# Kernel optimization log

Hardware: AMD Instinct MI355X
Metric: run time of the kernel (lower is better)

## Reference

```python
import jax, jax.numpy as jnp
import numpy as np

B, S, D, H = 2, 2048, 1024, 16
DK = D // H


def setup_inputs() -> dict:
    key = jax.random.key(0)
    ks = jax.random.split(key, 12)
    scale = 0.02
    inp = {
        "query": jax.random.normal(ks[0], (B, S, D), jnp.float32),
        "key_": jax.random.normal(ks[1], (B, S, D), jnp.float32),
        "value": jax.random.normal(ks[2], (B, S, D), jnp.float32),
        # causal mask; masked_fill where mask == 0
        "mask": jnp.tril(jnp.ones((S, S), jnp.int32))[None, None, :, :],
        # torch Linear weights are [out, in]; y = x @ W.T + b
        "Wq": jax.random.normal(ks[3], (D, D), jnp.float32) * scale,
        "bq": jax.random.normal(ks[4], (D,), jnp.float32) * scale,
        "Wk": jax.random.normal(ks[5], (D, D), jnp.float32) * scale,
        "bk": jax.random.normal(ks[6], (D,), jnp.float32) * scale,
        "Wv": jax.random.normal(ks[7], (D, D), jnp.float32) * scale,
        "bv": jax.random.normal(ks[8], (D,), jnp.float32) * scale,
        "Wo": jax.random.normal(ks[9], (D, D), jnp.float32) * scale,
        "bo": jax.random.normal(ks[10], (D,), jnp.float32) * scale,
    }
    return inp


def reference(query, key_, value, mask, Wq, bq, Wk, bk, Wv, bv, Wo, bo):
    # projections (torch Linear: x @ W.T + b)
    Q = query @ Wq.T + bq
    K = key_ @ Wk.T + bk
    V = value @ Wv.T + bv
    # [B, S, D] -> [B, H, S, DK]
    Q = Q.reshape(B, S, H, DK).transpose(0, 2, 1, 3)
    K = K.reshape(B, S, H, DK).transpose(0, 2, 1, 3)
    V = V.reshape(B, S, H, DK).transpose(0, 2, 1, 3)
    scores = jnp.einsum("bhqd,bhkd->bhqk", Q, K) / jnp.sqrt(jnp.float32(DK))
    scores = jnp.where(mask == 0, jnp.float32(-1e9), scores)
    attn = jax.nn.softmax(scores, axis=-1)
    # dropout is identity in eval mode
    context = jnp.einsum("bhqk,bhkd->bhqd", attn, V)
    context = context.transpose(0, 2, 1, 3).reshape(B, S, D)
    output = context @ Wo.T + bo
    return (output, attn)
```

## Files before the change

### kernel.cpp

```cpp
#include <hip/hip_runtime.h>
#include <hip/hip_bf16.h>

#define BB 2
#define SS 2048
#define DD 1024
#define HH 16

typedef __attribute__((ext_vector_type(8))) short bf16x8;
typedef __attribute__((ext_vector_type(4))) float f32x4;
typedef __attribute__((ext_vector_type(4))) unsigned int u32x4;

__device__ inline unsigned short f2bf(float f) {
  unsigned int u = __float_as_uint(f);
  u += 0x7fff + ((u >> 16) & 1);
  return (unsigned short)(u >> 16);
}

__device__ inline void gll16(const void* g, void* l) {
  __builtin_amdgcn_global_load_lds(
      (const __attribute__((address_space(1))) unsigned int*)g,
      (__attribute__((address_space(3))) unsigned int*)l, 16, 0, 0);
}

__device__ inline int swz(int row, int col) {
  return row * 64 + ((((col >> 3) + row + (row >> 3)) & 7) << 3) + (col & 7);
}

__global__ void convert_all(const float* __restrict__ q, const float* __restrict__ k,
                            const float* __restrict__ v, const float* __restrict__ wq,
                            const float* __restrict__ wk, const float* __restrict__ wv,
                            const float* __restrict__ wo, unsigned short* __restrict__ dst) {
  int gi = blockIdx.x * 256 + threadIdx.x;
  long base = (long)gi * 4;
  if (base >= 16777216L) return;
  const float* src;
  long off;
  if (base < 12582912L) {
    int a = (int)(base >> 22);
    off = base & 4194303L;
    src = (a == 0) ? q : (a == 1 ? k : v);
  } else {
    long wb = base - 12582912L;
    int a = (int)(wb >> 20);
    off = wb & 1048575L;
    src = (a == 0) ? wq : (a == 1 ? wk : (a == 2 ? wv : wo));
  }
  const float4 f = *(const float4*)(src + off);
  ushort4 o;
  o.x = f2bf(f.x); o.y = f2bf(f.y); o.z = f2bf(f.z); o.w = f2bf(f.w);
  *(ushort4*)(dst + base) = o;
}

template <int OUT_F32>
__global__ __launch_bounds__(256, 3) void gemm_bt(const unsigned short* __restrict__ Aall,
                                                  const unsigned short* __restrict__ Wall,
                                                  const float* __restrict__ b0,
                                                  const float* __restrict__ b1,
                                                  const float* __restrict__ b2,
                                                  void* __restrict__ Call) {
  __shared__ unsigned short As[128 * 64];
  __shared__ unsigned short Bs[128 * 64];
  const int tid = threadIdx.x;
  const int lane = tid & 63;
  const int w = tid >> 6;
  const int wm = w >> 1, wn = w & 1;
  const int z = blockIdx.z;
  const int m0 = blockIdx.y * 128;
  const int n0 = blockIdx.x * 128;
  const unsigned short* A = Aall + (long)z * 4194304;
  const unsigned short* W = Wall + (long)z * 1048576;
  const float* bias = (z == 0) ? b0 : (z == 1 ? b1 : b2);
  const int r = lane & 15, g = lane >> 4;
  const int lrow = lane >> 3;
  const int lcol = (lane & 7) * 8;

  f32x4 acc[4][4];
#pragma unroll
  for (int i = 0; i < 4; i++)
#pragma unroll
    for (int j = 0; j < 4; j++) acc[i][j] = (f32x4){0.f, 0.f, 0.f, 0.f};

  for (int kt = 0; kt < 16; kt++) {
    const int k0 = kt * 64;
#pragma unroll
    for (int t = 0; t < 4; t++) {
      int row = w * 32 + t * 8 + lrow;
      gll16(A + (long)(m0 + row) * 1024 + k0 + lcol, &As[(w * 32 + t * 8) * 64]);
      gll16(W + (long)(n0 + row) * 1024 + k0 + lcol, &Bs[(w * 32 + t * 8) * 64]);
    }
    __syncthreads();
#pragma unroll
    for (int kk = 0; kk < 2; kk++) {
      bf16x8 af[4], bfr[4];
#pragma unroll
      for (int mi = 0; mi < 4; mi++)
        af[mi] = *(const bf16x8*)&As[(wm * 64 + mi * 16 + r) * 64 + kk * 32 + g * 8];
#pragma unroll
      for (int ni = 0; ni < 4; ni++)
        bfr[ni] = *(const bf16x8*)&Bs[(wn * 64 + ni * 16 + r) * 64 + kk * 32 + g * 8];
#pragma unroll
      for (int mi = 0; mi < 4; mi++)
#pragma unroll
        for (int ni = 0; ni < 4; ni++)
          acc[mi][ni] = __builtin_amdgcn_mfma_f32_16x16x32_bf16(af[mi], bfr[ni], acc[mi][ni], 0, 0, 0);
    }
    __syncthreads();
  }
#pragma unroll
  for (int ni = 0; ni < 4; ni++) {
    int n = n0 + wn * 64 + ni * 16 + r;
    float bv = bias[n];
#pragma unroll
    for (int mi = 0; mi < 4; mi++) {
#pragma unroll
      for (int reg = 0; reg < 4; reg++) {
        int m = m0 + wm * 64 + mi * 16 + g * 4 + reg;
        float val = acc[mi][ni][reg] + bv;
        if (OUT_F32)
          ((float*)Call)[(long)m * 1024 + n] = val;
        else
          ((unsigned short*)Call)[(long)z * 4194304 + (long)m * 1024 + n] = f2bf(val);
      }
    }
  }
}

__global__ __launch_bounds__(256, 3) void attn_kernel(const unsigned short* __restrict__ Qb,
                                                      const unsigned short* __restrict__ Kb,
                                                      const unsigned short* __restrict__ Vb,
                                                      unsigned short* __restrict__ Ctx,
                                                      float* __restrict__ attn) {
  __shared__ unsigned short Qs[64 * 64];
  __shared__ unsigned short Ks[2][64 * 64];
  __shared__ unsigned short Vt[2][64 * 64];
  __shared__ unsigned short Ps[64 * 64];
  const int tid = threadIdx.x;
  const int lane = tid & 63;
  const int w = tid >> 6;
  const int r = lane & 15, g = lane >> 4;
  const int h = blockIdx.y, b = blockIdx.z;
  const int bh = b * HH + h;
  const unsigned short* Kg = Kb + (long)b * SS * DD + h * 64;
  const unsigned short* Vg = Vb + (long)b * SS * DD + h * 64;
  float* attn_bh = attn + (long)bh * SS * SS;
  const int srow = tid >> 3;
  const int scg = tid & 7;

  for (int half = 0; half < 2; half++) {
    const int qt = half ? (31 - (int)blockIdx.x) : (int)blockIdx.x;
    const int q0 = qt * 64;
    const unsigned short* Qg = Qb + (long)(b * SS + q0) * DD + h * 64;

    __syncthreads();
    u32x4 kpre[2];
#pragma unroll
    for (int it = 0; it < 2; it++) {
      int row = it * 32 + srow;
      *(u32x4*)&Qs[swz(row, scg * 8)] = *(const u32x4*)(Qg + (long)row * DD + scg * 8);
      kpre[it] = *(const u32x4*)(Kg + (long)row * DD + scg * 8);
    }
    __syncthreads();
    bf16x8 aq0 = *(const bf16x8*)&Qs[swz(16 * w + r, g * 8)];
    bf16x8 aq1 = *(const bf16x8*)&Qs[swz(16 * w + r, 32 + g * 8)];

    float rs[4] = {0.f, 0.f, 0.f, 0.f};
    for (int kt = 0; kt <= qt; kt++) {
      unsigned short* kbuf = Ks[kt & 1];
#pragma unroll
      for (int it = 0; it < 2; it++)
        *(u32x4*)&kbuf[swz(it * 32 + srow, scg * 8)] = kpre[it];
      const int ktn = (kt < qt) ? kt + 1 : kt;
#pragma unroll
      for (int it = 0; it < 2; it++)
        kpre[it] = *(const u32x4*)(Kg + (long)(ktn * 64 + it * 32 + srow) * DD + scg * 8);
      __syncthreads();
#pragma unroll
      for (int tj = 0; tj < 4; tj++) {
        bf16x8 bk0 = *(const bf16x8*)&kbuf[swz(tj * 16 + r, g * 8)];
        bf16x8 bk1 = *(const bf16x8*)&kbuf[swz(tj * 16 + r, 32 + g * 8)];
        f32x4 sa = (f32x4){0.f, 0.f, 0.f, 0.f};
        sa = __builtin_amdgcn_mfma_f32_16x16x32_bf16(aq0, bk0, sa, 0, 0, 0);
        sa = __builtin_amdgcn_mfma_f32_16x16x32_bf16(aq1, bk1, sa, 0, 0, 0);
        int colb = kt * 64 + tj * 16 + r;
        int rowb = q0 + 16 * w + g * 4;
#pragma unroll
        for (int reg = 0; reg < 4; reg++) {
          float p = (colb <= rowb + reg) ? __expf(sa[reg] * 0.125f) : 0.f;
          rs[reg] += p;
        }
      }
    }
#pragma unroll
    for (int reg = 0; reg < 4; reg++) {
#pragma unroll
      for (int m = 1; m <= 8; m <<= 1) rs[reg] += __shfl_xor(rs[reg], m);
    }
    float inv[4];
#pragma unroll
    for (int reg = 0; reg < 4; reg++) inv[reg] = 1.f / rs[reg];

    f32x4 oacc[4];
#pragma unroll
    for (int dj = 0; dj < 4; dj++) oacc[dj] = (f32x4){0.f, 0.f, 0.f, 0.f};
    u32x4 vpre[2];
#pragma unroll
    for (int it = 0; it < 2; it++) {
      int row = it * 32 + srow;
      kpre[it] = *(const u32x4*)(Kg + (long)row * DD + scg * 8);
      vpre[it] = *(const u32x4*)(Vg + (long)row * DD + scg * 8);
    }
    __syncthreads();
    for (int kt = 0; kt <= qt; kt++) {
      unsigned short* kbuf = Ks[kt & 1];
      unsigned short* vbuf = Vt[kt & 1];
#pragma unroll
      for (int it = 0; it < 2; it++) {
        *(u32x4*)&kbuf[swz(it * 32 + srow, scg * 8)] = kpre[it];
        union { u32x4 v4; unsigned short s[8]; } uv;
        uv.v4 = vpre[it];
#pragma unroll
        for (int i = 0; i < 8; i++) vbuf[swz(scg * 8 + i, it * 32 + srow)] = uv.s[i];
      }
      const int ktn = (kt < qt) ? kt + 1 : kt;
#pragma unroll
      for (int it = 0; it < 2; it++) {
        kpre[it] = *(const u32x4*)(Kg + (long)(ktn * 64 + it * 32 + srow) * DD + scg * 8);
        vpre[it] = *(const u32x4*)(Vg + (long)(ktn * 64 + it * 32 + srow) * DD + scg * 8);
      }
      __syncthreads();
#pragma unroll
      for (int tj = 0; tj < 4; tj++) {
        bf16x8 bk0 = *(const bf16x8*)&kbuf[swz(tj * 16 + r, g * 8)];
        bf16x8 bk1 = *(const bf16x8*)&kbuf[swz(tj * 16 + r, 32 + g * 8)];
        f32x4 sa = (f32x4){0.f, 0.f, 0.f, 0.f};
        sa = __builtin_amdgcn_mfma_f32_16x16x32_bf16(aq0, bk0, sa, 0, 0, 0);
        sa = __builtin_amdgcn_mfma_f32_16x16x32_bf16(aq1, bk1, sa, 0, 0, 0);
        int colb = kt * 64 + tj * 16 + r;
        int rowl = 16 * w + g * 4;
#pragma unroll
        for (int reg = 0; reg < 4; reg++) {
          int rowg = q0 + rowl + reg;
          float p = (colb <= rowg) ? __expf(sa[reg] * 0.125f) * inv[reg] : 0.f;
          attn_bh[(long)rowg * SS + colb] = p;
          Ps[swz(rowl + reg, tj * 16 + r)] = f2bf(p);
        }
      }
#pragma unroll
      for (int kk = 0; kk < 2; kk++) {
        bf16x8 ap = *(const bf16x8*)&Ps[swz(16 * w + r, kk * 32 + g * 8)];
#pragma unroll
        for (int dj = 0; dj < 4; dj++) {
          bf16x8 bv = *(const bf16x8*)&vbuf[swz(dj * 16 + r, kk * 32 + g * 8)];
          oacc[dj] = __builtin_amdgcn_mfma_f32_16x16x32_bf16(ap, bv, oacc[dj], 0, 0, 0);
        }
      }
    }
#pragma unroll
    for (int dj = 0; dj < 4; dj++) {
#pragma unroll
      for (int reg = 0; reg < 4; reg++) {
        int rowg = q0 + 16 * w + g * 4 + reg;
        Ctx[(long)(b * SS + rowg) * DD + h * 64 + dj * 16 + r] = f2bf(oacc[dj][reg]);
      }
    }
    int zs = (qt + 1) * 64;
    if (zs < SS) {
      int zc = SS - zs;
      f32x4 zero = (f32x4){0.f, 0.f, 0.f, 0.f};
      for (int rr = 0; rr < 64; rr++) {
        float* rp = attn_bh + (long)(q0 + rr) * SS + zs;
        for (int cc = tid * 4; cc < zc; cc += 1024) *(f32x4*)(rp + cc) = zero;
      }
    }
  }
}

extern "C" void kernel_launch(void* const* d_in, const int* in_sizes, int n_in,
                              void* d_out, int out_size, void* d_ws, size_t ws_size,
                              hipStream_t stream) {
  const float* q  = (const float*)d_in[0];
  const float* k  = (const float*)d_in[1];
  const float* v  = (const float*)d_in[2];
  const float* wq = (const float*)d_in[4];
  const float* bq = (const float*)d_in[5];
  const float* wk = (const float*)d_in[6];
  const float* bk = (const float*)d_in[7];
  const float* wv = (const float*)d_in[8];
  const float* bv = (const float*)d_in[9];
  const float* wo = (const float*)d_in[10];
  const float* bo = (const float*)d_in[11];

  unsigned short* ws = (unsigned short*)d_ws;
  unsigned short* Xq  = ws;
  unsigned short* Wqb = ws + 12582912;
  unsigned short* Qb  = ws + 16777216;
  unsigned short* Ctx = ws + 29360128;
  float* outp = (float*)d_out;
  float* attn = outp + 4194304;

  convert_all<<<dim3(16384), dim3(256), 0, stream>>>(q, k, v, wq, wk, wv, wo, ws);
  gemm_bt<0><<<dim3(8, 32, 3), dim3(256), 0, stream>>>(Xq, Wqb, bq, bk, bv, (void*)Qb);
  attn_kernel<<<dim3(16, 16, 2), dim3(256), 0, stream>>>(Qb, Qb + 4194304, Qb + 8388608, Ctx, attn);
  gemm_bt<1><<<dim3(8, 32, 1), dim3(256), 0, stream>>>(Ctx, Wqb + 3145728, bo, bo, bo, (void*)outp);
}
```

Baseline: 778.6 us.

## Compute transposed scores, load K/V straight from global, pre-transpose V in projection

The V projection epilogue now writes V transposed per batch-head, so the attention kernel can read V^T fragments directly from global memory. K and Q tiles are also read directly from global into MFMA operands, removing the LDS staging, double buffering and most barriers. Scores are computed as K·Q^T so each lane owns one query row; this makes the attention-probability stores contiguous float4 writes and turns the row-sum reduction into two shuffles. The costs are more uncached global traffic for repeated K/V reads, a lower occupancy hint in launch bounds, and no apparent barrier around the Ps reuse across iterations.

Result: slower. 858.6 us (+10.3%).

```diff
diff --git a/kernel.cpp b/kernel.cpp
--- a/kernel.cpp
+++ b/kernel.cpp
@@ -9,6 +9,7 @@
 typedef __attribute__((ext_vector_type(8))) short bf16x8;
 typedef __attribute__((ext_vector_type(4))) float f32x4;
 typedef __attribute__((ext_vector_type(4))) unsigned int u32x4;
+typedef __attribute__((ext_vector_type(2))) unsigned int u32x2;
 
 __device__ inline unsigned short f2bf(float f) {
   unsigned int u = __float_as_uint(f);
@@ -112,27 +113,38 @@
     float bv = bias[n];
 #pragma unroll
     for (int mi = 0; mi < 4; mi++) {
-#pragma unroll
-      for (int reg = 0; reg < 4; reg++) {
-        int m = m0 + wm * 64 + mi * 16 + g * 4 + reg;
-        float val = acc[mi][ni][reg] + bv;
-        if (OUT_F32)
-          ((float*)Call)[(long)m * 1024 + n] = val;
-        else
-          ((unsigned short*)Call)[(long)z * 4194304 + (long)m * 1024 + n] = f2bf(val);
-      }
-    }
-  }
-}
-
-__global__ __launch_bounds__(256, 3) void attn_kernel(const unsigned short* __restrict__ Qb,
+      if (OUT_F32) {
+#pragma unroll
+        for (int reg = 0; reg < 4; reg++) {
+          int m = m0 + wm * 64 + mi * 16 + g * 4 + reg;
+          ((float*)Call)[(long)m * 1024 + n] = acc[mi][ni][reg] + bv;
+        }
+      } else if (z == 2) {
+        int m = m0 + wm * 64 + mi * 16 + g * 4;
+        ushort4 o;
+        o.x = f2bf(acc[mi][ni][0] + bv);
+        o.y = f2bf(acc[mi][ni][1] + bv);
+        o.z = f2bf(acc[mi][ni][2] + bv);
+        o.w = f2bf(acc[mi][ni][3] + bv);
+        long idx = 2L * 4194304 + ((long)((m >> 11) * 1024 + n)) * 2048 + (m & 2047);
+        *(ushort4*)((unsigned short*)Call + idx) = o;
+      } else {
+#pragma unroll
+        for (int reg = 0; reg < 4; reg++) {
+          int m = m0 + wm * 64 + mi * 16 + g * 4 + reg;
+          ((unsigned short*)Call)[(long)z * 4194304 + (long)m * 1024 + n] =
+              f2bf(acc[mi][ni][reg] + bv);
+        }
+      }
+    }
+  }
+}
+
+__global__ __launch_bounds__(256, 2) void attn_kernel(const unsigned short* __restrict__ Qb,
                                                       const unsigned short* __restrict__ Kb,
-                                                      const unsigned short* __restrict__ Vb,
+                                                      const unsigned short* __restrict__ Vtg,
                                                       unsigned short* __restrict__ Ctx,
                                                       float* __restrict__ attn) {
-  __shared__ unsigned short Qs[64 * 64];
-  __shared__ unsigned short Ks[2][64 * 64];
-  __shared__ unsigned short Vt[2][64 * 64];
   __shared__ unsigned short Ps[64 * 64];
   const int tid = threadIdx.x;
   const int lane = tid & 63;
@@ -141,116 +153,73 @@
   const int h = blockIdx.y, b = blockIdx.z;
   const int bh = b * HH + h;
   const unsigned short* Kg = Kb + (long)b * SS * DD + h * 64;
-  const unsigned short* Vg = Vb + (long)b * SS * DD + h * 64;
+  const unsigned short* Vg = Vtg + (long)bh * 64 * SS;
   float* attn_bh = attn + (long)bh * SS * SS;
-  const int srow = tid >> 3;
-  const int scg = tid & 7;
 
   for (int half = 0; half < 2; half++) {
     const int qt = half ? (31 - (int)blockIdx.x) : (int)blockIdx.x;
     const int q0 = qt * 64;
     const unsigned short* Qg = Qb + (long)(b * SS + q0) * DD + h * 64;
-
-    __syncthreads();
-    u32x4 kpre[2];
-#pragma unroll
-    for (int it = 0; it < 2; it++) {
-      int row = it * 32 + srow;
-      *(u32x4*)&Qs[swz(row, scg * 8)] = *(const u32x4*)(Qg + (long)row * DD + scg * 8);
-      kpre[it] = *(const u32x4*)(Kg + (long)row * DD + scg * 8);
-    }
-    __syncthreads();
-    bf16x8 aq0 = *(const bf16x8*)&Qs[swz(16 * w + r, g * 8)];
-    bf16x8 aq1 = *(const bf16x8*)&Qs[swz(16 * w + r, 32 + g * 8)];
-
-    float rs[4] = {0.f, 0.f, 0.f, 0.f};
+    bf16x8 aq0 = *(const bf16x8*)(Qg + (long)(16 * w + r) * DD + g * 8);
+    bf16x8 aq1 = *(const bf16x8*)(Qg + (long)(16 * w + r) * DD + 32 + g * 8);
+
+    float rs = 0.f;
     for (int kt = 0; kt <= qt; kt++) {
-      unsigned short* kbuf = Ks[kt & 1];
-#pragma unroll
-      for (int it = 0; it < 2; it++)
-        *(u32x4*)&kbuf[swz(it * 32 + srow, scg * 8)] = kpre[it];
-      const int ktn = (kt < qt) ? kt + 1 : kt;
-#pragma unroll
-      for (int it = 0; it < 2; it++)
-        kpre[it] = *(const u32x4*)(Kg + (long)(ktn * 64 + it * 32 + srow) * DD + scg * 8);
-      __syncthreads();
-#pragma unroll
-      for (int tj = 0; tj < 4; tj++) {
-        bf16x8 bk0 = *(const bf16x8*)&kbuf[swz(tj * 16 + r, g * 8)];
-        bf16x8 bk1 = *(const bf16x8*)&kbuf[swz(tj * 16 + r, 32 + g * 8)];
+      const unsigned short* Kt = Kg + (long)kt * 64 * DD;
+#pragma unroll
+      for (int mi = 0; mi < 4; mi++) {
+        bf16x8 ak0 = *(const bf16x8*)(Kt + (long)(mi * 16 + r) * DD + g * 8);
+        bf16x8 ak1 = *(const bf16x8*)(Kt + (long)(mi * 16 + r) * DD + 32 + g * 8);
         f32x4 sa = (f32x4){0.f, 0.f, 0.f, 0.f};
-        sa = __builtin_amdgcn_mfma_f32_16x16x32_bf16(aq0, bk0, sa, 0, 0, 0);
-        sa = __builtin_amdgcn_mfma_f32_16x16x32_bf16(aq1, bk1, sa, 0, 0, 0);
-        int colb = kt * 64 + tj * 16 + r;
-        int rowb = q0 + 16 * w + g * 4;
-#pragma unroll
-        for (int reg = 0; reg < 4; reg++) {
-          float p = (colb <= rowb + reg) ? __expf(sa[reg] * 0.125f) : 0.f;
-          rs[reg] += p;
-        }
-      }
-    }
-#pragma unroll
-    for (int reg = 0; reg < 4; reg++) {
-#pragma unroll
-      for (int m = 1; m <= 8; m <<= 1) rs[reg] += __shfl_xor(rs[reg], m);
-    }
-    float inv[4];
-#pragma unroll
-    for (int reg = 0; reg < 4; reg++) inv[reg] = 1.f / rs[reg];
+        sa = __builtin_amdgcn_mfma_f32_16x16x32_bf16(ak0, aq0, sa, 0, 0, 0);
+        sa = __builtin_amdgcn_mfma_f32_16x16x32_bf16(ak1, aq1, sa, 0, 0, 0);
+        if (kt == qt) {
+#pragma unroll
+          for (int reg = 0; reg < 4; reg++)
+            rs += (mi * 16 + g * 4 + reg <= 16 * w + r) ? __expf(sa[reg] * 0.125f) : 0.f;
+        } else {
+#pragma unroll
+          for (int reg = 0; reg < 4; reg++) rs += __expf(sa[reg] * 0.125f);
+        }
+      }
+    }
+    rs += __shfl_xor(rs, 16);
+    rs += __shfl_xor(rs, 32);
+    const float inv = 1.f / rs;
 
     f32x4 oacc[4];
 #pragma unroll
     for (int dj = 0; dj < 4; dj++) oacc[dj] = (f32x4){0.f, 0.f, 0.f, 0.f};
-    u32x4 vpre[2];
-#pragma unroll
-    for (int it = 0; it < 2; it++) {
-      int row = it * 32 + srow;
-      kpre[it] = *(const u32x4*)(Kg + (long)row * DD + scg * 8);
-      vpre[it] = *(const u32x4*)(Vg + (long)row * DD + scg * 8);
-    }
-    __syncthreads();
+    float* rowp = attn_bh + (long)(q0 + 16 * w + r) * SS;
     for (int kt = 0; kt <= qt; kt++) {
-      unsigned short* kbuf = Ks[kt & 1];
-      unsigned short* vbuf = Vt[kt & 1];
-#pragma unroll
-      for (int it = 0; it < 2; it++) {
-        *(u32x4*)&kbuf[swz(it * 32 + srow, scg * 8)] = kpre[it];
-        union { u32x4 v4; unsigned short s[8]; } uv;
-        uv.v4 = vpre[it];
-#pragma unroll
-        for (int i = 0; i < 8; i++) vbuf[swz(scg * 8 + i, it * 32 + srow)] = uv.s[i];
-      }
-      const int ktn = (kt < qt) ? kt + 1 : kt;
-#pragma unroll
-      for (int it = 0; it < 2; it++) {
-        kpre[it] = *(const u32x4*)(Kg + (long)(ktn * 64 + it * 32 + srow) * DD + scg * 8);
-        vpre[it] = *(const u32x4*)(Vg + (long)(ktn * 64 + it * 32 + srow) * DD + scg * 8);
-      }
-      __syncthreads();
-#pragma unroll
-      for (int tj = 0; tj < 4; tj++) {
-        bf16x8 bk0 = *(const bf16x8*)&kbuf[swz(tj * 16 + r, g * 8)];
-        bf16x8 bk1 = *(const bf16x8*)&kbuf[swz(tj * 16 + r, 32 + g * 8)];
+      const unsigned short* Kt = Kg + (long)kt * 64 * DD;
+#pragma unroll
+      for (int mi = 0; mi < 4; mi++) {
+        bf16x8 ak0 = *(const bf16x8*)(Kt + (long)(mi * 16 + r) * DD + g * 8);
+        bf16x8 ak1 = *(const bf16x8*)(Kt + (long)(mi * 16 + r) * DD + 32 + g * 8);
         f32x4 sa = (f32x4){0.f, 0.f, 0.f, 0.f};
-        sa = __builtin_amdgcn_mfma_f32_16x16x32_bf16(aq0, bk0, sa, 0, 0, 0);
-        sa = __builtin_amdgcn_mfma_f32_16x16x32_bf16(aq1, bk1, sa, 0, 0, 0);
-        int colb = kt * 64 + tj * 16 + r;
-        int rowl = 16 * w + g * 4;
-#pragma unroll
-        for (int reg = 0; reg < 4; reg++) {
-          int rowg = q0 + rowl + reg;
-          float p = (colb <= rowg) ? __expf(sa[reg] * 0.125f) * inv[reg] : 0.f;
-          attn_bh[(long)rowg * SS + colb] = p;
-          Ps[swz(rowl + reg, tj * 16 + r)] = f2bf(p);
-        }
+        sa = __builtin_amdgcn_mfma_f32_16x16x32_bf16(ak0, aq0, sa, 0, 0, 0);
+        sa = __builtin_amdgcn_mfma_f32_16x16x32_bf16(ak1, aq1, sa, 0, 0, 0);
+        f32x4 p;
+        if (kt == qt) {
+#pragma unroll
+          for (int reg = 0; reg < 4; reg++)
+            p[reg] = (mi * 16 + g * 4 + reg <= 16 * w + r) ? __expf(sa[reg] * 0.125f) * inv : 0.f;
+        } else {
+#pragma unroll
+          for (int reg = 0; reg < 4; reg++) p[reg] = __expf(sa[reg] * 0.125f) * inv;
+        }
+        *(f32x4*)(rowp + kt * 64 + mi * 16 + g * 4) = p;
+        unsigned int p01 = (unsigned)f2bf(p[0]) | ((unsigned)f2bf(p[1]) << 16);
+        unsigned int p23 = (unsigned)f2bf(p[2]) | ((unsigned)f2bf(p[3]) << 16);
+        *(u32x2*)&Ps[swz(16 * w + r, mi * 16 + g * 4)] = (u32x2){p01, p23};
       }
 #pragma unroll
       for (int kk = 0; kk < 2; kk++) {
         bf16x8 ap = *(const bf16x8*)&Ps[swz(16 * w + r, kk * 32 + g * 8)];
 #pragma unroll
         for (int dj = 0; dj < 4; dj++) {
-          bf16x8 bv = *(const bf16x8*)&vbuf[swz(dj * 16 + r, kk * 32 + g * 8)];
+          bf16x8 bv = *(const bf16x8*)(Vg + (long)(dj * 16 + r) * SS + kt * 64 + kk * 32 + g * 8);
           oacc[dj] = __builtin_amdgcn_mfma_f32_16x16x32_bf16(ap, bv, oacc[dj], 0, 0, 0);
         }
       }
```
